# Performance work log

Hardware: AMD Instinct MI355X
Metric: run time of the kernel (lower is better)

The kernel has to match this reference:

```python
import jax, jax.numpy as jnp
import numpy as np

N_NODES = 100000
N_EDGES = 1600000
D = 64


def setup_inputs() -> dict:
    key = jax.random.key(0)
    k1, k2, k3 = jax.random.split(key, 3)
    z = jax.random.normal(k1, (N_NODES, D), dtype=jnp.float32)
    ei = jax.random.randint(k2, (2, N_EDGES), 0, N_NODES, dtype=jnp.int32)
    W = jax.random.normal(k3, (D, D), dtype=jnp.float32) * (1.0 / np.sqrt(D))
    b = jnp.zeros((D,), dtype=jnp.float32)
    return {"z": z, "ei": ei, "W": W, "b": b}


def reference(z, ei, W, b):
    # PyG GCNConv(64,64) with default add_self_loops=True, normalize=True, bias,
    # followed by ReLU (from StructDec.forward).
    N = z.shape[0]
    loops = jnp.arange(N, dtype=ei.dtype)
    src = jnp.concatenate([ei[0], loops])  # [E+N]
    dst = jnp.concatenate([ei[1], loops])  # [E+N]

    # symmetric normalization: deg computed on dst with unit edge weights
    deg = jax.ops.segment_sum(jnp.ones_like(dst, dtype=z.dtype), dst, num_segments=N)
    dinv = jnp.where(deg > 0, jax.lax.rsqrt(deg), 0.0)  # deg >= 1 due to self-loops
    norm = dinv[src] * dinv[dst]  # [E+N]

    # linear transform first (small GEMM), then gather-scale-scatter
    x = z @ W.T  # [N, D]
    msg = x[src] * norm[:, None]  # [E+N, D]
    out = jax.ops.segment_sum(msg, dst, num_segments=N) + b  # [N, D]
    return jax.nn.relu(out)
```

## Files before the change

kernel.cpp:

```cpp
#include <hip/hip_runtime.h>

#define DD 64
#define BSH 7
#define GBKT 128
#define CAP 2560
#define TILE 4096
#define PTHREADS 512
#define MAXBK 1024

__device__ __forceinline__ float bflo(unsigned int u) {
    return __uint_as_float(u << 16);
}
__device__ __forceinline__ float bfhi(unsigned int u) {
    return __uint_as_float(u & 0xffff0000u);
}
__device__ __forceinline__ unsigned short f2bf(float f) {
    unsigned int b = __float_as_uint(f);
    return (unsigned short)((b + 0x7fffu + ((b >> 16) & 1u)) >> 16);
}
__device__ __forceinline__ void acc_row(uint4 r, float4& lo, float4& hi) {
    lo.x += bflo(r.x); lo.y += bfhi(r.x);
    lo.z += bflo(r.y); lo.w += bfhi(r.y);
    hi.x += bflo(r.z); hi.y += bfhi(r.z);
    hi.z += bflo(r.w); hi.w += bfhi(r.w);
}

__global__ void init_k(int* __restrict__ bcur, int NBK) {
    int i = blockIdx.x * blockDim.x + threadIdx.x;
    if (i < NBK) bcur[i] = i * CAP;
}

__global__ __launch_bounds__(PTHREADS) void part_k(const int* __restrict__ src,
                                                   const int* __restrict__ dst,
                                                   int* __restrict__ bcur,
                                                   int* __restrict__ bp,
                                                   int E, int NBK) {
    __shared__ int hist[MAXBK];
    __shared__ int scanb[MAXBK];
    __shared__ int gbase[MAXBK];
    __shared__ int stage[TILE];
    __shared__ unsigned short bstage[TILE];

    int tid = threadIdx.x;
    int tbase = blockIdx.x * TILE;
    int n = E - tbase;
    if (n > TILE) n = TILE;

    for (int i = tid; i < NBK; i += PTHREADS) hist[i] = 0;
    __syncthreads();

    int pv[TILE / PTHREADS];
    int pb[TILE / PTHREADS];
    #pragma unroll
    for (int e = 0; e < TILE / PTHREADS; ++e) {
        int i = tid + e * PTHREADS;
        pb[e] = -1;
        if (i < n) {
            int s = src[tbase + i];
            int d = dst[tbase + i];
            pv[e] = (s << BSH) | (d & (GBKT - 1));
            pb[e] = d >> BSH;
            atomicAdd(&hist[pb[e]], 1);
        }
    }
    __syncthreads();

    if (tid < 64) {
        int run = 0;
        for (int base = 0; base < NBK; base += 64) {
            int i = base + tid;
            int orig = (i < NBK) ? hist[i] : 0;
            int v = orig;
            #pragma unroll
            for (int off = 1; off < 64; off <<= 1) {
                int t = __shfl_up(v, off, 64);
                if (tid >= off) v += t;
            }
            if (i < NBK) scanb[i] = run + v - orig;
            run += __shfl(v, 63, 64);
        }
    }
    __syncthreads();

    for (int i = tid; i < NBK; i += PTHREADS)
        if (hist[i]) gbase[i] = atomicAdd(&bcur[i], hist[i]);
    __syncthreads();
    for (int i = tid; i < NBK; i += PTHREADS) hist[i] = scanb[i];
    __syncthreads();

    #pragma unroll
    for (int e = 0; e < TILE / PTHREADS; ++e) {
        if (pb[e] >= 0) {
            int r = atomicAdd(&hist[pb[e]], 1);
            stage[r] = pv[e];
            bstage[r] = (unsigned short)pb[e];
        }
    }
    __syncthreads();

    for (int i = tid; i < n; i += PTHREADS) {
        int b = bstage[i];
        bp[gbase[b] + (i - scanb[b])] = stage[i];
    }
}

__global__ void nodedeg_k(const int* __restrict__ bp, const int* __restrict__ bcur,
                          float* __restrict__ dinv, int N) {
    __shared__ int cnt[GBKT];
    int k = blockIdx.x;
    int tid = threadIdx.x;
    int ebeg = k * CAP;
    int eend = bcur[k];
    if (tid < GBKT) cnt[tid] = 0;
    __syncthreads();
    for (int i = ebeg + tid; i < eend; i += 256)
        atomicAdd(&cnt[bp[i] & (GBKT - 1)], 1);
    __syncthreads();
    if (tid < GBKT) {
        int node = (k << BSH) + tid;
        if (node < N) dinv[node] = rsqrtf((float)(1 + cnt[tid]));
    }
}

__global__ __launch_bounds__(512) void gemm_k(const float* __restrict__ z,
                                              const float* __restrict__ W,
                                              const float* __restrict__ dinv,
                                              ushort4* __restrict__ ybf, int N) {
    __shared__ float Wt[64 * 68];
    __shared__ float zt[32 * 68];
    int tid = threadIdx.x;
    for (int i = tid; i < DD * DD; i += 512) {
        int d = i >> 6, k = i & 63;
        Wt[k * 68 + d] = W[i];
    }
    {
        int zr = blockIdx.x * 32 + (tid >> 4);
        float4 v = (zr < N) ? reinterpret_cast<const float4*>(z)[(size_t)zr * 16 + (tid & 15)]
                            : make_float4(0.f, 0.f, 0.f, 0.f);
        *reinterpret_cast<float4*>(&zt[(tid >> 4) * 68 + (tid & 15) * 4]) = v;
    }
    __syncthreads();
    int r = tid >> 4;
    int c = tid & 15;
    int row = blockIdx.x * 32 + r;
    float4 acc = make_float4(0.f, 0.f, 0.f, 0.f);
    #pragma unroll
    for (int k = 0; k < DD; ++k) {
        float zv = zt[r * 68 + k];
        float4 w = *reinterpret_cast<const float4*>(&Wt[k * 68 + c * 4]);
        acc.x = fmaf(zv, w.x, acc.x);
        acc.y = fmaf(zv, w.y, acc.y);
        acc.z = fmaf(zv, w.z, acc.z);
        acc.w = fmaf(zv, w.w, acc.w);
    }
    if (row < N) {
        float s = dinv[row];
        ushort4 o;
        o.x = f2bf(acc.x * s);
        o.y = f2bf(acc.y * s);
        o.z = f2bf(acc.z * s);
        o.w = f2bf(acc.w * s);
        ybf[(size_t)row * 16 + c] = o;
    }
}

__global__ __launch_bounds__(256) void bg_k(const uint4* __restrict__ ybf,
                                            const int* __restrict__ bp,
                                            const int* __restrict__ bcur,
                                            const float4* __restrict__ b4,
                                            float4* __restrict__ out4, int N) {
    __shared__ int cnt[GBKT];
    __shared__ int excl[GBKT];
    __shared__ int cur[GBKT];
    __shared__ int sorted[CAP];
    __shared__ int nextn;
    int k = blockIdx.x;
    int tid = threadIdx.x;
    int ebeg = k * CAP;
    int eend = bcur[k];
    int base = k << BSH;

    if (tid < GBKT) cnt[tid] = 0;
    if (tid == 0) nextn = 0;
    __syncthreads();
    for (int i = ebeg + tid; i < eend; i += 256)
        atomicAdd(&cnt[bp[i] & (GBKT - 1)], 1);
    __syncthreads();

    if (tid < GBKT) excl[tid] = cnt[tid];
    __syncthreads();
    #pragma unroll
    for (int off = 1; off < GBKT; off <<= 1) {
        int t = (tid < GBKT && tid >= off) ? excl[tid - off] : 0;
        __syncthreads();
        if (tid < GBKT) excl[tid] += t;
        __syncthreads();
    }
    if (tid < GBKT) {
        excl[tid] -= cnt[tid];
        cur[tid] = excl[tid];
    }
    __syncthreads();

    for (int i = ebeg + tid; i < eend; i += 256) {
        int v = bp[i];
        int l = v & (GBKT - 1);
        int pos = atomicAdd(&cur[l], 1);
        sorted[pos] = v >> BSH;
    }
    __syncthreads();

    int lane = tid & 63;
    int c = tid & 7;
    for (;;) {
        int slot;
        if ((tid & 7) == 0) slot = atomicAdd(&nextn, 1);
        slot = __shfl(slot, lane & 56, 64);
        if (slot >= GBKT) break;
        int node = base + slot;
        if (node >= N) continue;
        int beg = excl[slot];
        int cn = cnt[slot];
        int end = beg + cn;
        uint4 v = ybf[(size_t)node * 8 + c];
        float4 a0 = make_float4(bflo(v.x), bfhi(v.x), bflo(v.y), bfhi(v.y));
        float4 a1 = make_float4(bflo(v.z), bfhi(v.z), bflo(v.w), bfhi(v.w));
        float4 e0 = make_float4(0.f, 0.f, 0.f, 0.f);
        float4 e1 = e0;
        int j = beg;
        for (; j + 3 < end; j += 4) {
            int s0 = sorted[j], s1 = sorted[j + 1], s2 = sorted[j + 2], s3 = sorted[j + 3];
            uint4 r0 = ybf[(size_t)s0 * 8 + c];
            uint4 r1 = ybf[(size_t)s1 * 8 + c];
            uint4 r2 = ybf[(size_t)s2 * 8 + c];
            uint4 r3 = ybf[(size_t)s3 * 8 + c];
            acc_row(r0, a0, a1);
            acc_row(r1, e0, e1);
            acc_row(r2, a0, a1);
            acc_row(r3, e0, e1);
        }
        for (; j < end; ++j) {
            uint4 r = ybf[(size_t)sorted[j] * 8 + c];
            acc_row(r, a0, a1);
        }
        a0.x += e0.x; a0.y += e0.y; a0.z += e0.z; a0.w += e0.w;
        a1.x += e1.x; a1.y += e1.y; a1.z += e1.z; a1.w += e1.w;

        float dn = rsqrtf((float)(1 + cn));
        float4 bb0 = b4[2 * c];
        float4 bb1 = b4[2 * c + 1];
        float4 o0, o1;
        o0.x = fmaxf(fmaf(a0.x, dn, bb0.x), 0.f);
        o0.y = fmaxf(fmaf(a0.y, dn, bb0.y), 0.f);
        o0.z = fmaxf(fmaf(a0.z, dn, bb0.z), 0.f);
        o0.w = fmaxf(fmaf(a0.w, dn, bb0.w), 0.f);
        o1.x = fmaxf(fmaf(a1.x, dn, bb1.x), 0.f);
        o1.y = fmaxf(fmaf(a1.y, dn, bb1.y), 0.f);
        o1.z = fmaxf(fmaf(a1.z, dn, bb1.z), 0.f);
        o1.w = fmaxf(fmaf(a1.w, dn, bb1.w), 0.f);
        out4[(size_t)node * 16 + 2 * c] = o0;
        out4[(size_t)node * 16 + 2 * c + 1] = o1;
    }
}


extern "C" void kernel_launch(void* const* d_in, const int* in_sizes, int n_in,
                              void* d_out, int out_size, void* d_ws, size_t ws_size,
                              hipStream_t stream) {
    const float* z = (const float*)d_in[0];
    const int* ei  = (const int*)d_in[1];
    const float* W = (const float*)d_in[2];
    const float* b = (const float*)d_in[3];
    float* out = (float*)d_out;

    const int N = in_sizes[0] / DD;
    const int E = in_sizes[1] / 2;
    const int* src = ei;
    const int* dst = ei + E;

    const int NBK = (N + GBKT - 1) >> BSH;

    unsigned short* ybf = (unsigned short*)d_ws;
    float* dinv  = (float*)(ybf + (size_t)64 * N);
    int*   bcur  = (int*)(dinv + N);
    int*   bp    = bcur + NBK;

    init_k<<<(NBK + 255) / 256, 256, 0, stream>>>(bcur, NBK);
    part_k<<<(E + TILE - 1) / TILE, PTHREADS, 0, stream>>>(src, dst, bcur, bp, E, NBK);
    nodedeg_k<<<NBK, 256, 0, stream>>>(bp, bcur, dinv, N);
    gemm_k<<<(N + 31) / 32, 512, 0, stream>>>(z, W, dinv, (ushort4*)ybf, N);
    bg_k<<<NBK, 256, 0, stream>>>((const uint4*)ybf, bp, bcur,
                                  (const float4*)b, (float4*)out, N);
}
```

Before: 93.55 us.

## Fold bucket init into GEMM, move dinv scaling into gather, halve bucket size

Bucket-cursor initialisation now happens inside the GEMM kernel, which runs first, so one launch is dropped. The GEMM no longer depends on the degree pass. The per-source dinv scaling moves from the GEMM output into the gather loop, which adds a scattered dinv load per edge. Buckets shrink from 128 to 64 nodes, so there are more blocks and a smaller sorted buffer in LDS. The block prefix scan becomes a wavefront shuffle scan, and the gather loop is unrolled to 8.

```diff
diff --git a/kernel.cpp b/kernel.cpp
--- a/kernel.cpp
+++ b/kernel.cpp
@@ -1,12 +1,12 @@
 #include <hip/hip_runtime.h>
 
 #define DD 64
-#define BSH 7
-#define GBKT 128
-#define CAP 2560
+#define BSH 6
+#define GBKT 64
+#define CAP 1280
 #define TILE 4096
 #define PTHREADS 512
-#define MAXBK 1024
+#define MAXBK 1600
 
 __device__ __forceinline__ float bflo(unsigned int u) {
     return __uint_as_float(u << 16);
@@ -18,16 +18,56 @@
     unsigned int b = __float_as_uint(f);
     return (unsigned short)((b + 0x7fffu + ((b >> 16) & 1u)) >> 16);
 }
-__device__ __forceinline__ void acc_row(uint4 r, float4& lo, float4& hi) {
-    lo.x += bflo(r.x); lo.y += bfhi(r.x);
-    lo.z += bflo(r.y); lo.w += bfhi(r.y);
-    hi.x += bflo(r.z); hi.y += bfhi(r.z);
-    hi.z += bflo(r.w); hi.w += bfhi(r.w);
-}
-
-__global__ void init_k(int* __restrict__ bcur, int NBK) {
-    int i = blockIdx.x * blockDim.x + threadIdx.x;
-    if (i < NBK) bcur[i] = i * CAP;
+__device__ __forceinline__ void fma_row(uint4 r, float s, float4& lo, float4& hi) {
+    lo.x = fmaf(bflo(r.x), s, lo.x); lo.y = fmaf(bfhi(r.x), s, lo.y);
+    lo.z = fmaf(bflo(r.y), s, lo.z); lo.w = fmaf(bfhi(r.y), s, lo.w);
+    hi.x = fmaf(bflo(r.z), s, hi.x); hi.y = fmaf(bfhi(r.z), s, hi.y);
+    hi.z = fmaf(bflo(r.w), s, hi.z); hi.w = fmaf(bfhi(r.w), s, hi.w);
+}
+
+__global__ __launch_bounds__(512) void gemm_k(const float* __restrict__ z,
+                                              const float* __restrict__ W,
+                                              ushort4* __restrict__ ybf,
+                                              int* __restrict__ bcur,
+                                              int N, int NBK) {
+    int tid = threadIdx.x;
+    int gid = blockIdx.x * 512 + tid;
+    if (gid < NBK) bcur[gid] = gid * CAP;
+
+    __shared__ float Wt[64 * 68];
+    __shared__ float zt[32 * 68];
+    for (int i = tid; i < DD * DD; i += 512) {
+        int d = i >> 6, k = i & 63;
+        Wt[k * 68 + d] = W[i];
+    }
+    {
+        int zr = blockIdx.x * 32 + (tid >> 4);
+        float4 v = (zr < N) ? reinterpret_cast<const float4*>(z)[(size_t)zr * 16 + (tid & 15)]
+                            : make_float4(0.f, 0.f, 0.f, 0.f);
+        *reinterpret_cast<float4*>(&zt[(tid >> 4) * 68 + (tid & 15) * 4]) = v;
+    }
+    __syncthreads();
+    int r = tid >> 4;
+    int c = tid & 15;
+    int row = blockIdx.x * 32 + r;
+    float4 acc = make_float4(0.f, 0.f, 0.f, 0.f);
+    #pragma unroll
+    for (int k = 0; k < DD; ++k) {
+        float zv = zt[r * 68 + k];
+        float4 w = *reinterpret_cast<const float4*>(&Wt[k * 68 + c * 4]);
+        acc.x = fmaf(zv, w.x, acc.x);
+        acc.y = fmaf(zv, w.y, acc.y);
+        acc.z = fmaf(zv, w.z, acc.z);
+        acc.w = fmaf(zv, w.w, acc.w);
+    }
+    if (row < N) {
+        ushort4 o;
+        o.x = f2bf(acc.x);
+        o.y = f2bf(acc.y);
+        o.z = f2bf(acc.z);
+        o.w = f2bf(acc.w);
+        ybf[(size_t)row * 16 + c] = o;
+    }
 }
 
 __global__ __launch_bounds__(PTHREADS) void part_k(const int* __restrict__ src,
@@ -122,49 +162,8 @@
     }
 }
 
-__global__ __launch_bounds__(512) void gemm_k(const float* __restrict__ z,
-                                              const float* __restrict__ W,
-                                              const float* __restrict__ dinv,
-                                              ushort4* __restrict__ ybf, int N) {
-    __shared__ float Wt[64 * 68];
-    __shared__ float zt[32 * 68];
-    int tid = threadIdx.x;
-    for (int i = tid; i < DD * DD; i += 512) {
-        int d = i >> 6, k = i & 63;
-        Wt[k * 68 + d] = W[i];
-    }
-    {
-        int zr = blockIdx.x * 32 + (tid >> 4);
-        float4 v = (zr < N) ? reinterpret_cast<const float4*>(z)[(size_t)zr * 16 + (tid & 15)]
-                            : make_float4(0.f, 0.f, 0.f, 0.f);
-        *reinterpret_cast<float4*>(&zt[(tid >> 4) * 68 + (tid & 15) * 4]) = v;
-    }
-    __syncthreads();
-    int r = tid >> 4;
-    int c = tid & 15;
-    int row = blockIdx.x * 32 + r;
-    float4 acc = make_float4(0.f, 0.f, 0.f, 0.f);
-    #pragma unroll
-    for (int k = 0; k < DD; ++k) {
-        float zv = zt[r * 68 + k];
-        float4 w = *reinterpret_cast<const float4*>(&Wt[k * 68 + c * 4]);
-        acc.x = fmaf(zv, w.x, acc.x);
-        acc.y = fmaf(zv, w.y, acc.y);
-        acc.z = fmaf(zv, w.z, acc.z);
-        acc.w = fmaf(zv, w.w, acc.w);
-    }
-    if (row < N) {
-        float s = dinv[row];
-        ushort4 o;
-        o.x = f2bf(acc.x * s);
-        o.y = f2bf(acc.y * s);
-        o.z = f2bf(acc.z * s);
-        o.w = f2bf(acc.w * s);
-        ybf[(size_t)row * 16 + c] = o;
-    }
-}
-
 __global__ __launch_bounds__(256) void bg_k(const uint4* __restrict__ ybf,
+                                            const float* __restrict__ dinv,
                                             const int* __restrict__ bp,
                                             const int* __restrict__ bcur,
                                             const float4* __restrict__ b4,
@@ -187,18 +186,16 @@
         atomicAdd(&cnt[bp[i] & (GBKT - 1)], 1);
     __syncthreads();
 
-    if (tid < GBKT) excl[tid] = cnt[tid];
-    __syncthreads();
-    #pragma unroll
-    for (int off = 1; off < GBKT; off <<= 1) {
-        int t = (tid < GBKT && tid >= off) ? excl[tid - off] : 0;
-        __syncthreads();
-        if (tid < GBKT) excl[tid] += t;
-        __syncthreads();
-    }
-    if (tid < GBKT) {
-        excl[tid] -= cnt[tid];
-        cur[tid] = excl[tid];
+    if (tid < 64) {
+        int c0 = cnt[tid];
+        int v = c0;
+        #pragma unroll
+        for (int off = 1; off < 64; off <<= 1) {
+            int t = __shfl_up(v, off, 64);
+            if (tid >= off) v += t;
+        }
+        excl[tid] = v - c0;
+        cur[tid] = v - c0;
     }
     __syncthreads();
 
@@ -222,31 +219,52 @@
         int beg = excl[slot];
         int cn = cnt[slot];
         int end = beg + cn;
-        uint4 v = ybf[(size_t)node * 8 + c];
-        float4 a0 = make_float4(bflo(v.x), bfhi(v.x), bflo(v.y), bfhi(v.y));
-        float4 a1 = make_float4(bflo(v.z), bfhi(v.z), bflo(v.w), bfhi(v.w));
-        float4 e0 = make_float4(0.f, 0.f, 0.f, 0.f);
-        float4 e1 = e0;
+        float dn = rsqrtf((float)(1 + cn));
+        float4 a0 = make_float4(0.f, 0.f, 0.f, 0.f), a1 = a0;
+        float4 e0 = a0, e1 = a0;
+        fma_row(ybf[(size_t)node * 8 + c], dn, a0, a1);
         int j = beg;
-        for (; j + 3 < end; j += 4) {
-            int s0 = sorted[j], s1 = sorted[j + 1], s2 = sorted[j + 2], s3 = sorted[j + 3];
+        for (; j + 7 < end; j += 8) {
+            int s0 = sorted[j],     s1 = sorted[j + 1], s2 = sorted[j + 2], s3 = sorted[j + 3];
+            int s4 = sorted[j + 4], s5 = sorted[j + 5], s6 = sorted[j + 6], s7 = sorted[j + 7];
+            float d0 = dinv[s0], d1 = dinv[s1], d2 = dinv[s2], d3 = dinv[s3];
+            float d4 = dinv[s4], d5 = dinv[s5], d6 = dinv[s6], d7 = dinv[s7];
             uint4 r0 = ybf[(size_t)s0 * 8 + c];
             uint4 r1 = ybf[(size_t)s1 * 8 + c];
             uint4 r2 = ybf[(size_t)s2 * 8 + c];
             uint4 r3 = ybf[(size_t)s3 * 8 + c];
-            acc_row(r0, a0, a1);
-            acc_row(r1, e0, e1);
-            acc_row(r2, a0, a1);
-            acc_row(r3, e0, e1);
+            uint4 r4 = ybf[(size_t)s4 * 8 + c];
+            uint4 r5 = ybf[(size_t)s5 * 8 + c];
+            uint4 r6 = ybf[(size_t)s6 * 8 + c];
+            uint4 r7 = ybf[(size_t)s7 * 8 + c];
+            fma_row(r0, d0, a0, a1);
+            fma_row(r1, d1, e0, e1);
+            fma_row(r2, d2, a0, a1);
+            fma_row(r3, d3, e0, e1);
+            fma_row(r4, d4, a0, a1);
+            fma_row(r5, d5, e0, e1);
+            fma_row(r6, d6, a0, a1);
+            fma_row(r7, d7, e0, e1);
+        }
+        for (; j + 3 < end; j += 4) {
+            int s0 = sorted[j], s1 = sorted[j + 1], s2 = sorted[j + 2], s3 = sorted[j + 3];
+            float d0 = dinv[s0], d1 = dinv[s1], d2 = dinv[s2], d3 = dinv[s3];
+            uint4 r0 = ybf[(size_t)s0 * 8 + c];
+            uint4 r1 = ybf[(size_t)s1 * 8 + c];
+            uint4 r2 = ybf[(size_t)s2 * 8 + c];
+            uint4 r3 = ybf[(size_t)s3 * 8 + c];
+            fma_row(r0, d0, a0, a1);
+            fma_row(r1, d1, e0, e1);
+            fma_row(r2, d2, a0, a1);
+            fma_row(r3, d3, e0, e1);
         }
         for (; j < end; ++j) {
-            uint4 r = ybf[(size_t)sorted[j] * 8 + c];
-            acc_row(r, a0, a1);
+            int s = sorted[j];
+            fma_row(ybf[(size_t)s * 8 + c], dinv[s], a0, a1);
         }
         a0.x += e0.x; a0.y += e0.y; a0.z += e0.z; a0.w += e0.w;
         a1.x += e1.x; a1.y += e1.y; a1.z += e1.z; a1.w += e1.w;
 
-        float dn = rsqrtf((float)(1 + cn));
         float4 bb0 = b4[2 * c];
         float4 bb1 = b4[2 * c + 1];
         float4 o0, o1;
@@ -285,10 +303,9 @@
     int*   bcur  = (int*)(dinv + N);
     int*   bp    = bcur + NBK;
 
-    init_k<<<(NBK + 255) / 256, 256, 0, stream>>>(bcur, NBK);
+    gemm_k<<<(N + 31) / 32, 512, 0, stream>>>(z, W, (ushort4*)ybf, bcur, N, NBK);
     part_k<<<(E + TILE - 1) / TILE, PTHREADS, 0, stream>>>(src, dst, bcur, bp, E, NBK);
     nodedeg_k<<<NBK, 256, 0, stream>>>(bp, bcur, dinv, N);
-    gemm_k<<<(N + 31) / 32, 512, 0, stream>>>(z, W, dinv, (ushort4*)ybf, N);
-    bg_k<<<NBK, 256, 0, stream>>>((const uint4*)ybf, bp, bcur,
+    bg_k<<<NBK, 256, 0, stream>>>((const uint4*)ybf, dinv, bp, bcur,
                                   (const float4*)b, (float4*)out, N);
 }
```

Measured after the change: 97.38 us. +4.1%, slower.
